# Performance work log

Hardware: AMD Instinct MI355X
Metric: run time of the kernel (lower is better)

The kernel has to match this reference:

```python
import jax, jax.numpy as jnp
import numpy as np

N = 100000
D = 128
E = 1600000


def _glorot(key, shape):
    fan_in, fan_out = shape[1], shape[0]
    lim = float(np.sqrt(6.0 / (fan_in + fan_out)))
    return jax.random.uniform(key, shape, jnp.float32, -lim, lim)


def setup_inputs() -> dict:
    key = jax.random.key(0)
    ks = jax.random.split(key, 12)
    x = jax.random.normal(ks[0], (N, D), jnp.float32)
    edge_index = jax.random.randint(ks[1], (2, E), 0, N, jnp.int64)
    edge_weight = jax.random.uniform(ks[2], (E,), jnp.float32)
    params = {}
    for i, layer in enumerate(["1", "2", "3"]):
        params[f"W{layer}l"] = _glorot(ks[3 + 3 * i], (D, D))
        params[f"b{layer}"] = jnp.zeros((D,), jnp.float32)
        params[f"W{layer}r"] = _glorot(ks[4 + 3 * i], (D, D))
    return {"x": x, "edge_index": edge_index, "edge_weight": edge_weight, **params}


def _sage_layer(x, src, dst, Wl, b, Wr):
    # mean aggregation of source-node features onto target nodes
    deg = jax.ops.segment_sum(jnp.ones((src.shape[0],), x.dtype), dst, num_segments=N)
    agg = jax.ops.segment_sum(x[src], dst, num_segments=N)  # [N, D]
    agg = agg / jnp.maximum(deg, 1.0)[:, None]
    # SAGEConv: lin_l(agg) + lin_r(x); bias only on lin_l. Then relu.
    out = agg @ Wl.T + b + x @ Wr.T
    return jax.nn.relu(out)  # Dropout is identity in eval mode


def reference(x, edge_index, edge_weight, W1l, b1, W1r, W2l, b2, W2r, W3l, b3, W3r):
    src, dst = edge_index[0], edge_index[1]
    h = _sage_layer(x, src, dst, W1l, b1, W1r)
    h = _sage_layer(h, src, dst, W2l, b2, W2r)
    h = _sage_layer(h, src, dst, W3l, b3, W3r)
    return h
```

## Files before the change

kernel.cpp:

```cpp
#include <hip/hip_runtime.h>

#define NN 100000
#define DD 128
#define EE 1600000
#define CAP 64
#define NGROUP 8
#define NPX (NN / NGROUP)

typedef __attribute__((ext_vector_type(8))) short short8;
typedef __attribute__((ext_vector_type(4))) float f32x4;

__device__ __forceinline__ unsigned short f2bf(float f) {
  unsigned int u = __builtin_bit_cast(unsigned int, f);
  unsigned int r = (u + 0x7FFFu + ((u >> 16) & 1u)) >> 16;
  return (unsigned short)r;
}
__device__ __forceinline__ float bf2f(unsigned int lo16) {
  unsigned int u = lo16 << 16;
  return __builtin_bit_cast(float, u);
}


__global__ __launch_bounds__(256) void cast_x_kernel(const float* __restrict__ x,
                                                     unsigned short* __restrict__ xb) {
  int i = blockIdx.x * 256 + threadIdx.x;
  if (i < NN * DD / 4) {
    float4 v = ((const float4*)x)[i];
    ushort4 o;
    o.x = f2bf(v.x); o.y = f2bf(v.y); o.z = f2bf(v.z); o.w = f2bf(v.w);
    ((ushort4*)xb)[i] = o;
  }
}

__global__ __launch_bounds__(256) void cast_w_kernel(
    const float* __restrict__ W0, const float* __restrict__ W1,
    const float* __restrict__ W2, const float* __restrict__ W3,
    const float* __restrict__ W4, const float* __restrict__ W5,
    unsigned short* __restrict__ wb) {
  int i = blockIdx.x * 256 + threadIdx.x;
  if (i >= 6 * DD * DD / 4) return;
  int m = i >> 12;
  const float* Ws[6] = {W0, W1, W2, W3, W4, W5};
  float4 v = ((const float4*)Ws[m])[i & 4095];
  ushort4 o;
  o.x = f2bf(v.x); o.y = f2bf(v.y); o.z = f2bf(v.z); o.w = f2bf(v.w);
  ((ushort4*)wb)[i] = o;
}


__global__ __launch_bounds__(256) void fill2_kernel(const int* __restrict__ ei,
                                                    int* __restrict__ cnt,
                                                    int* __restrict__ csr) {
  const int g = blockIdx.x & (NGROUP - 1);
  const int bs = blockIdx.x >> 3;
  const int lo = g * NPX, hi = lo + NPX;
  const int stride = (gridDim.x >> 3) * 256;
  for (int e = bs * 256 + threadIdx.x; e < EE; e += stride) {
    int d = ei[EE + e];
    if (d >= lo && d < hi) {
      int s = ei[e];
      int slot = atomicAdd(&cnt[d], 1);
      if (slot < CAP) csr[(size_t)d * CAP + slot] = s;
    }
  }
}


__global__ __launch_bounds__(256) void agg_kernel(const unsigned short* __restrict__ hb,
                                                  const int* __restrict__ cnt,
                                                  const int* __restrict__ csr,
                                                  unsigned short* __restrict__ aggb) {
  const int node = blockIdx.x * 4 + (threadIdx.x >> 6);
  const int lane = threadIdx.x & 63;
  if (node >= NN) return;
  const int n = min(cnt[node], CAP);
  const int* __restrict__ lst = csr + (size_t)node * CAP;
  const unsigned int* __restrict__ hp = (const unsigned int*)hb;
  float ax = 0.f, ay = 0.f;
  int p = 0;
  for (; p + 4 <= n; p += 4) {
    int s0 = lst[p], s1 = lst[p + 1], s2 = lst[p + 2], s3 = lst[p + 3];
    unsigned int v0 = hp[(size_t)s0 * 64 + lane];
    unsigned int v1 = hp[(size_t)s1 * 64 + lane];
    unsigned int v2 = hp[(size_t)s2 * 64 + lane];
    unsigned int v3 = hp[(size_t)s3 * 64 + lane];
    ax += bf2f(v0 & 0xffff) + bf2f(v1 & 0xffff) + bf2f(v2 & 0xffff) + bf2f(v3 & 0xffff);
    ay += bf2f(v0 >> 16) + bf2f(v1 >> 16) + bf2f(v2 >> 16) + bf2f(v3 >> 16);
  }
  for (; p < n; ++p) {
    unsigned int v = hp[(size_t)lst[p] * 64 + lane];
    ax += bf2f(v & 0xffff);
    ay += bf2f(v >> 16);
  }
  const float inv = 1.0f / fmaxf((float)n, 1.0f);
  unsigned int out = (unsigned int)f2bf(ax * inv) | ((unsigned int)f2bf(ay * inv) << 16);
  ((unsigned int*)aggb)[(size_t)node * 64 + lane] = out;
}


template <int OUT_F32>
__global__ __launch_bounds__(256, 2) void lin_mfma_kernel(
    const unsigned short* __restrict__ hb, const unsigned short* __restrict__ aggb,
    const unsigned short* __restrict__ Wl, const unsigned short* __restrict__ Wr,
    const float* __restrict__ bias, void* __restrict__ outp) {
  __shared__ short8 lw[2][DD * DD / 8];
  const int t = threadIdx.x;
  const int w = t >> 6;
  const int l = t & 63;
  const int lr = l & 15;
  const int kq = l >> 4;
  const int n0 = blockIdx.x * 128;

  {
    const short8* gl = (const short8*)Wl;
    const short8* gr = (const short8*)Wr;
    for (int i = t; i < DD * DD / 8; i += 256) {
      int j = i >> 4, c = i & 15;
      int dst = j * 16 + (c ^ (j & 15));
      lw[0][dst] = gl[i];
      lw[1][dst] = gr[i];
    }
  }

  short8 ag[2][4], ah[2][4];
#pragma unroll
  for (int rt = 0; rt < 2; ++rt) {
    int arow = n0 + w * 32 + rt * 16 + lr;
    if (arow >= NN) arow = NN - 1;
#pragma unroll
    for (int kk = 0; kk < 4; ++kk) {
      ag[rt][kk] = *(const short8*)(aggb + (size_t)arow * DD + kk * 32 + kq * 8);
      ah[rt][kk] = *(const short8*)(hb + (size_t)arow * DD + kk * 32 + kq * 8);
    }
  }
  __syncthreads();

#pragma unroll
  for (int ct = 0; ct < 8; ++ct) {
    const int j = ct * 16 + lr;
    short8 bl[4], br[4];
#pragma unroll
    for (int kk = 0; kk < 4; ++kk) {
      int c = kk * 4 + kq;
      int src = j * 16 + (c ^ (j & 15));
      bl[kk] = lw[0][src];
      br[kk] = lw[1][src];
    }
    const float bv = bias[j];
#pragma unroll
    for (int rt = 0; rt < 2; ++rt) {
      f32x4 acc = {0.f, 0.f, 0.f, 0.f};
#pragma unroll
      for (int kk = 0; kk < 4; ++kk)
        acc = __builtin_amdgcn_mfma_f32_16x16x32_bf16(ag[rt][kk], bl[kk], acc, 0, 0, 0);
#pragma unroll
      for (int kk = 0; kk < 4; ++kk)
        acc = __builtin_amdgcn_mfma_f32_16x16x32_bf16(ah[rt][kk], br[kk], acc, 0, 0, 0);
#pragma unroll
      for (int r = 0; r < 4; ++r) {
        const int row = n0 + w * 32 + rt * 16 + kq * 4 + r;
        if (row < NN) {
          float v = fmaxf(acc[r] + bv, 0.f);
          if (OUT_F32)
            ((float*)outp)[(size_t)row * DD + j] = v;
          else
            ((unsigned short*)outp)[(size_t)row * DD + j] = f2bf(v);
        }
      }
    }
  }
}


extern "C" void kernel_launch(void* const* d_in, const int* in_sizes, int n_in,
                              void* d_out, int out_size, void* d_ws, size_t ws_size,
                              hipStream_t stream) {
  const float* x = (const float*)d_in[0];
  const int* ei = (const int*)d_in[1];
  const float* W1l = (const float*)d_in[3];
  const float* b1 = (const float*)d_in[4];
  const float* W1r = (const float*)d_in[5];
  const float* W2l = (const float*)d_in[6];
  const float* b2 = (const float*)d_in[7];
  const float* W2r = (const float*)d_in[8];
  const float* W3l = (const float*)d_in[9];
  const float* b3 = (const float*)d_in[10];
  const float* W3r = (const float*)d_in[11];
  float* out = (float*)d_out;

  char* ws = (char*)d_ws;
  size_t off = 0;
  auto alloc = [&](size_t bytes) {
    void* p = ws + off;
    off += (bytes + 255) & ~(size_t)255;
    return p;
  };
  int* cnt = (int*)alloc(NN * sizeof(int));
  int* csr = (int*)alloc((size_t)NN * CAP * sizeof(int));
  unsigned short* hbA = (unsigned short*)alloc((size_t)NN * DD * 2);
  unsigned short* hbB = (unsigned short*)alloc((size_t)NN * DD * 2);
  unsigned short* aggb = (unsigned short*)alloc((size_t)NN * DD * 2);
  unsigned short* wb = (unsigned short*)alloc(6 * DD * DD * 2);

  unsigned short* w1l = wb + 0 * DD * DD;
  unsigned short* w1r = wb + 1 * DD * DD;
  unsigned short* w2l = wb + 2 * DD * DD;
  unsigned short* w2r = wb + 3 * DD * DD;
  unsigned short* w3l = wb + 4 * DD * DD;
  unsigned short* w3r = wb + 5 * DD * DD;

  cast_x_kernel<<<(NN * DD / 4 + 255) / 256, 256, 0, stream>>>(x, hbA);
  cast_w_kernel<<<(6 * DD * DD / 4 + 255) / 256, 256, 0, stream>>>(
      W1l, W1r, W2l, W2r, W3l, W3r, wb);

  hipMemsetAsync(cnt, 0, NN * sizeof(int), stream);
  fill2_kernel<<<NGROUP * 256, 256, 0, stream>>>(ei, cnt, csr);

  const int LIN_GRID = (NN + 127) / 128;
  agg_kernel<<<NN / 4, 256, 0, stream>>>(hbA, cnt, csr, aggb);
  lin_mfma_kernel<0><<<LIN_GRID, 256, 0, stream>>>(hbA, aggb, w1l, w1r, b1, hbB);
  agg_kernel<<<NN / 4, 256, 0, stream>>>(hbB, cnt, csr, aggb);
  lin_mfma_kernel<0><<<LIN_GRID, 256, 0, stream>>>(hbB, aggb, w2l, w2r, b2, hbA);
  agg_kernel<<<NN / 4, 256, 0, stream>>>(hbA, cnt, csr, aggb);
  lin_mfma_kernel<1><<<LIN_GRID, 256, 0, stream>>>(hbA, aggb, w3l, w3r, b3, out);
}
```

Measured before the change: 398.0 us.

## Vectorize CSR fill reads, use 16-byte gathers in aggregation, double linear tile rows

The CSR fill kernel now reads destination indices as int4 and handles four edges per thread. The aggregation kernel splits each wavefront into four sub-groups of 16 lanes. Each sub-group gathers a full neighbor row with 16-byte loads, and the partial sums are combined with cross-lane shuffles. The linear MFMA kernel processes 256 rows per block instead of 128, so the staged weights are reused over more rows, at the cost of more registers and fewer blocks.

```diff
diff --git a/kernel.cpp b/kernel.cpp
--- a/kernel.cpp
+++ b/kernel.cpp
@@ -54,13 +54,26 @@
   const int g = blockIdx.x & (NGROUP - 1);
   const int bs = blockIdx.x >> 3;
   const int lo = g * NPX, hi = lo + NPX;
-  const int stride = (gridDim.x >> 3) * 256;
-  for (int e = bs * 256 + threadIdx.x; e < EE; e += stride) {
-    int d = ei[EE + e];
-    if (d >= lo && d < hi) {
-      int s = ei[e];
-      int slot = atomicAdd(&cnt[d], 1);
-      if (slot < CAP) csr[(size_t)d * CAP + slot] = s;
+  const int tpg = (gridDim.x >> 3) * 256;
+  const int4* __restrict__ d4 = (const int4*)(ei + EE);
+  for (int q = bs * 256 + threadIdx.x; q < EE / 4; q += tpg) {
+    const int4 d = d4[q];
+    const int e = q * 4;
+    if (d.x >= lo && d.x < hi) {
+      int slot = atomicAdd(&cnt[d.x], 1);
+      if (slot < CAP) csr[(size_t)d.x * CAP + slot] = ei[e];
+    }
+    if (d.y >= lo && d.y < hi) {
+      int slot = atomicAdd(&cnt[d.y], 1);
+      if (slot < CAP) csr[(size_t)d.y * CAP + slot] = ei[e + 1];
+    }
+    if (d.z >= lo && d.z < hi) {
+      int slot = atomicAdd(&cnt[d.z], 1);
+      if (slot < CAP) csr[(size_t)d.z * CAP + slot] = ei[e + 2];
+    }
+    if (d.w >= lo && d.w < hi) {
+      int slot = atomicAdd(&cnt[d.w], 1);
+      if (slot < CAP) csr[(size_t)d.w * CAP + slot] = ei[e + 3];
     }
   }
 }
@@ -72,29 +85,53 @@
                                                   unsigned short* __restrict__ aggb) {
   const int node = blockIdx.x * 4 + (threadIdx.x >> 6);
   const int lane = threadIdx.x & 63;
-  if (node >= NN) return;
+  const int sub = lane >> 4;
+  const int cl = lane & 15;
   const int n = min(cnt[node], CAP);
   const int* __restrict__ lst = csr + (size_t)node * CAP;
-  const unsigned int* __restrict__ hp = (const unsigned int*)hb;
-  float ax = 0.f, ay = 0.f;
-  int p = 0;
-  for (; p + 4 <= n; p += 4) {
-    int s0 = lst[p], s1 = lst[p + 1], s2 = lst[p + 2], s3 = lst[p + 3];
-    unsigned int v0 = hp[(size_t)s0 * 64 + lane];
-    unsigned int v1 = hp[(size_t)s1 * 64 + lane];
-    unsigned int v2 = hp[(size_t)s2 * 64 + lane];
-    unsigned int v3 = hp[(size_t)s3 * 64 + lane];
-    ax += bf2f(v0 & 0xffff) + bf2f(v1 & 0xffff) + bf2f(v2 & 0xffff) + bf2f(v3 & 0xffff);
-    ay += bf2f(v0 >> 16) + bf2f(v1 >> 16) + bf2f(v2 >> 16) + bf2f(v3 >> 16);
-  }
-  for (; p < n; ++p) {
-    unsigned int v = hp[(size_t)lst[p] * 64 + lane];
-    ax += bf2f(v & 0xffff);
-    ay += bf2f(v >> 16);
-  }
-  const float inv = 1.0f / fmaxf((float)n, 1.0f);
-  unsigned int out = (unsigned int)f2bf(ax * inv) | ((unsigned int)f2bf(ay * inv) << 16);
-  ((unsigned int*)aggb)[(size_t)node * 64 + lane] = out;
+  float acc[8] = {0.f, 0.f, 0.f, 0.f, 0.f, 0.f, 0.f, 0.f};
+
+  int p = sub;
+  for (; p + 4 < n; p += 8) {
+    const int s0 = lst[p];
+    const int s1 = lst[p + 4];
+    const uint4 v0 = *(const uint4*)(hb + (size_t)s0 * DD + cl * 8);
+    const uint4 v1 = *(const uint4*)(hb + (size_t)s1 * DD + cl * 8);
+    acc[0] += bf2f(v0.x & 0xffff) + bf2f(v1.x & 0xffff);
+    acc[1] += bf2f(v0.x >> 16) + bf2f(v1.x >> 16);
+    acc[2] += bf2f(v0.y & 0xffff) + bf2f(v1.y & 0xffff);
+    acc[3] += bf2f(v0.y >> 16) + bf2f(v1.y >> 16);
+    acc[4] += bf2f(v0.z & 0xffff) + bf2f(v1.z & 0xffff);
+    acc[5] += bf2f(v0.z >> 16) + bf2f(v1.z >> 16);
+    acc[6] += bf2f(v0.w & 0xffff) + bf2f(v1.w & 0xffff);
+    acc[7] += bf2f(v0.w >> 16) + bf2f(v1.w >> 16);
+  }
+  if (p < n) {
+    const int s0 = lst[p];
+    const uint4 v0 = *(const uint4*)(hb + (size_t)s0 * DD + cl * 8);
+    acc[0] += bf2f(v0.x & 0xffff);
+    acc[1] += bf2f(v0.x >> 16);
+    acc[2] += bf2f(v0.y & 0xffff);
+    acc[3] += bf2f(v0.y >> 16);
+    acc[4] += bf2f(v0.z & 0xffff);
+    acc[5] += bf2f(v0.z >> 16);
+    acc[6] += bf2f(v0.w & 0xffff);
+    acc[7] += bf2f(v0.w >> 16);
+  }
+#pragma unroll
+  for (int i = 0; i < 8; ++i) {
+    acc[i] += __shfl_xor(acc[i], 16, 64);
+    acc[i] += __shfl_xor(acc[i], 32, 64);
+  }
+  if (sub == 0) {
+    const float inv = 1.0f / fmaxf((float)n, 1.0f);
+    uint4 o;
+    o.x = (unsigned int)f2bf(acc[0] * inv) | ((unsigned int)f2bf(acc[1] * inv) << 16);
+    o.y = (unsigned int)f2bf(acc[2] * inv) | ((unsigned int)f2bf(acc[3] * inv) << 16);
+    o.z = (unsigned int)f2bf(acc[4] * inv) | ((unsigned int)f2bf(acc[5] * inv) << 16);
+    o.w = (unsigned int)f2bf(acc[6] * inv) | ((unsigned int)f2bf(acc[7] * inv) << 16);
+    *(uint4*)(aggb + (size_t)node * DD + cl * 8) = o;
+  }
 }
 
 
@@ -109,7 +146,7 @@
   const int l = t & 63;
   const int lr = l & 15;
   const int kq = l >> 4;
-  const int n0 = blockIdx.x * 128;
+  const int n0 = blockIdx.x * 256;
 
   {
     const short8* gl = (const short8*)Wl;
@@ -122,10 +159,10 @@
     }
   }
 
-  short8 ag[2][4], ah[2][4];
-#pragma unroll
-  for (int rt = 0; rt < 2; ++rt) {
-    int arow = n0 + w * 32 + rt * 16 + lr;
+  short8 ag[4][4], ah[4][4];
+#pragma unroll
+  for (int rt = 0; rt < 4; ++rt) {
+    int arow = n0 + w * 64 + rt * 16 + lr;
     if (arow >= NN) arow = NN - 1;
 #pragma unroll
     for (int kk = 0; kk < 4; ++kk) {
@@ -148,7 +185,7 @@
     }
     const float bv = bias[j];
 #pragma unroll
-    for (int rt = 0; rt < 2; ++rt) {
+    for (int rt = 0; rt < 4; ++rt) {
       f32x4 acc = {0.f, 0.f, 0.f, 0.f};
 #pragma unroll
       for (int kk = 0; kk < 4; ++kk)
@@ -158,7 +195,7 @@
         acc = __builtin_amdgcn_mfma_f32_16x16x32_bf16(ah[rt][kk], br[kk], acc, 0, 0, 0);
 #pragma unroll
       for (int r = 0; r < 4; ++r) {
-        const int row = n0 + w * 32 + rt * 16 + kq * 4 + r;
+        const int row = n0 + w * 64 + rt * 16 + kq * 4 + r;
         if (row < NN) {
           float v = fmaxf(acc[r] + bv, 0.f);
           if (OUT_F32)
@@ -216,7 +253,7 @@
   hipMemsetAsync(cnt, 0, NN * sizeof(int), stream);
   fill2_kernel<<<NGROUP * 256, 256, 0, stream>>>(ei, cnt, csr);
 
-  const int LIN_GRID = (NN + 127) / 128;
+  const int LIN_GRID = (NN + 255) / 256;
   agg_kernel<<<NN / 4, 256, 0, stream>>>(hbA, cnt, csr, aggb);
   lin_mfma_kernel<0><<<LIN_GRID, 256, 0, stream>>>(hbA, aggb, w1l, w1r, b1, hbB);
   agg_kernel<<<NN / 4, 256, 0, stream>>>(hbB, cnt, csr, aggb);
```

Result: faster. 356.0 us (-10.6%).
